# Performance work log

Hardware: AMD Instinct MI355X
Metric: run time of the kernel (lower is better)

Reference implementation:

```python
import jax, jax.numpy as jnp
import numpy as np

N, E, G = 50000, 800000, 64          # nodes, edges, graphs
IN, HID, OUT, H = 256, 64, 64, 4     # input dim, per-head hidden, output dim, heads
NEG_SLOPE = 0.2                      # PyG GATConv leaky_relu slope


def _lin(k, fan_in, fan_out):
    return jax.random.normal(k, (fan_in, fan_out), jnp.float32) * (1.0 / np.sqrt(fan_in))


def setup_inputs() -> dict:
    key = jax.random.key(0)
    ks = jax.random.split(key, 16)
    x = jax.random.normal(ks[0], (N, IN), jnp.float32)
    edge_index = jax.random.randint(ks[1], (2, E), 0, N, dtype=jnp.int32)
    batch = jnp.sort(jax.random.randint(ks[2], (N,), 0, G, dtype=jnp.int32))
    # layer 1: IN -> H x HID (concat)
    W1 = _lin(ks[3], IN, H * HID)
    a_src1 = jax.random.normal(ks[4], (H, HID), jnp.float32) * 0.1
    a_dst1 = jax.random.normal(ks[5], (H, HID), jnp.float32) * 0.1
    b1 = jnp.zeros((H * HID,), jnp.float32)
    # layer 2: H*HID -> H x HID (concat)
    W2 = _lin(ks[6], H * HID, H * HID)
    a_src2 = jax.random.normal(ks[7], (H, HID), jnp.float32) * 0.1
    a_dst2 = jax.random.normal(ks[8], (H, HID), jnp.float32) * 0.1
    b2 = jnp.zeros((H * HID,), jnp.float32)
    W3 = _lin(ks[9], H * HID, OUT)
    a_src3 = jax.random.normal(ks[10], (1, OUT), jnp.float32) * 0.1
    a_dst3 = jax.random.normal(ks[11], (1, OUT), jnp.float32) * 0.1
    b3 = jnp.zeros((OUT,), jnp.float32)
    return {"x": x, "edge_index": edge_index, "batch": batch,
            "W1": W1, "a_src1": a_src1, "a_dst1": a_dst1, "b1": b1,
            "W2": W2, "a_src2": a_src2, "a_dst2": a_dst2, "b2": b2,
            "W3": W3, "a_src3": a_src3, "a_dst3": a_dst3, "b3": b3}


def gat_conv(x, src, dst, W, a_src, a_dst, b, heads, out_ch):
    """PyG-style GATConv (eval mode, concat=True semantics; heads=1 == no concat)."""
    n = x.shape[0]
    h = (x @ W).reshape(n, heads, out_ch)                     # [N,H,C]
    alpha_s = jnp.sum(h * a_src, axis=-1)                     # [N,H]
    alpha_d = jnp.sum(h * a_dst, axis=-1)                     # [N,H]
    e = jax.nn.leaky_relu(alpha_s[src] + alpha_d[dst], NEG_SLOPE)  # [E',H]
    # segment softmax over destination nodes (self-loops guarantee nonempty segments)
    m = jax.ops.segment_max(e, dst, num_segments=n)
    e = jnp.exp(e - m[dst])
    denom = jax.ops.segment_sum(e, dst, num_segments=n)
    alpha = e / (denom[dst] + 1e-16)                          # [E',H]
    msg = h[src] * alpha[:, :, None]                          # [E',H,C]
    out = jax.ops.segment_sum(msg, dst, num_segments=n)       # [N,H,C]
    return out.reshape(n, heads * out_ch) + b


def reference(x, edge_index, batch, W1, a_src1, a_dst1, b1, W2, a_src2, a_dst2, b2,
              W3, a_src3, a_dst3, b3):
    n = x.shape[0]
    # GATConv default add_self_loops=True
    loops = jnp.arange(n, dtype=edge_index.dtype)
    src = jnp.concatenate([edge_index[0], loops])
    dst = jnp.concatenate([edge_index[1], loops])

    h = gat_conv(x, src, dst, W1, a_src1, a_dst1, b1, H, HID)
    h = jax.nn.elu(h)  # dropout disabled in eval
    h = gat_conv(h, src, dst, W2, a_src2, a_dst2, b2, H, HID)
    h = jax.nn.elu(h)
    node_embeddings = gat_conv(h, src, dst, W3, a_src3, a_dst3, b3, 1, OUT)

    # global_mean_pool over batch ids
    sums = jax.ops.segment_sum(node_embeddings, batch, num_segments=G)
    counts = jax.ops.segment_sum(jnp.ones((n,), node_embeddings.dtype), batch, num_segments=G)
    graph_embeddings = sums / jnp.maximum(counts, 1.0)[:, None]
    return node_embeddings, graph_embeddings
```

## Files before the change

### kernel.cpp

```cpp
#include <hip/hip_runtime.h>
#include <hip/hip_bf16.h>
#include <hip/hip_fp16.h>

typedef __attribute__((ext_vector_type(8))) _Float16 f16x8;
typedef __attribute__((ext_vector_type(4))) _Float16 f16x4;
typedef __attribute__((ext_vector_type(4))) float f32x4;

static __device__ __forceinline__ void st(float* p, float v)  { *p = v; }
static __device__ __forceinline__ void st(__half* p, float v) { *p = __float2half(v); }

static __device__ __forceinline__ void splitf16(float v, __half& hi, __half& lo) {
    hi = __float2half(v);
    lo = __float2half(v - __half2float(hi));
}

__global__ void k_hist(const int* __restrict__ ei, int* deg, int E) {
    int e = blockIdx.x * blockDim.x + threadIdx.x;
    if (e < E) atomicAdd(&deg[ei[E + e]], 1);
}

__global__ void k_scan1(const int* __restrict__ deg, int* __restrict__ offs,
                        int* __restrict__ bsum, int N) {
    __shared__ int sh[256];
    int i = blockIdx.x * 256 + threadIdx.x;
    int v = (i < N) ? (deg[i] + 1) : 0;
    sh[threadIdx.x] = v;
    __syncthreads();
#pragma unroll
    for (int off = 1; off < 256; off <<= 1) {
        int t = (threadIdx.x >= off) ? sh[threadIdx.x - off] : 0;
        __syncthreads();
        sh[threadIdx.x] += t;
        __syncthreads();
    }
    if (i < N) offs[i] = sh[threadIdx.x] - v;
    if (threadIdx.x == 255) bsum[blockIdx.x] = sh[255];
}

__global__ void k_scan2(int* __restrict__ bsum, int nb) {
    __shared__ int sh[256];
    int v = (threadIdx.x < nb) ? bsum[threadIdx.x] : 0;
    sh[threadIdx.x] = v;
    __syncthreads();
#pragma unroll
    for (int off = 1; off < 256; off <<= 1) {
        int t = (threadIdx.x >= off) ? sh[threadIdx.x - off] : 0;
        __syncthreads();
        sh[threadIdx.x] += t;
        __syncthreads();
    }
    if (threadIdx.x < nb) bsum[threadIdx.x] = sh[threadIdx.x] - v;
    if (threadIdx.x == 255) bsum[nb] = sh[255];
}

__global__ void k_scan3(int* __restrict__ offs, int* __restrict__ cursor,
                        const int* __restrict__ bsum, int N, int nb) {
    int i = blockIdx.x * 256 + threadIdx.x;
    if (i < N) {
        int v = offs[i] + bsum[blockIdx.x];
        offs[i] = v;
        cursor[i] = v;
    }
    if (i == 0) offs[N] = bsum[nb];
}

__global__ void k_scatter_all(const int* __restrict__ ei, int* cursor, int* csr,
                              int E, int N) {
    int e = blockIdx.x * blockDim.x + threadIdx.x;
    if (e < E) {
        int d = ei[E + e];
        int p = atomicAdd(&cursor[d], 1);
        csr[p] = ei[e];
    } else if (e < E + N) {
        int i = e - E;
        int p = atomicAdd(&cursor[i], 1);
        csr[p] = i;
    }
}

__global__ void k_wsplit_all(const float* __restrict__ W1, const float* __restrict__ W2,
                             const float* __restrict__ W3,
                             __half* __restrict__ w1h, __half* __restrict__ w1l,
                             __half* __restrict__ w2h, __half* __restrict__ w2l,
                             __half* __restrict__ w3h, __half* __restrict__ w3l) {
    int idx = blockIdx.x * 256 + threadIdx.x;
    const float* W; __half *Wh, *Wl; int M, base;
    constexpr int K = 256;
    if (idx < 65536)       { W = W1; Wh = w1h; Wl = w1l; M = 256; base = idx; }
    else if (idx < 131072) { W = W2; Wh = w2h; Wl = w2l; M = 256; base = idx - 65536; }
    else if (idx < 147456) { W = W3; Wh = w3h; Wl = w3l; M = 64;  base = idx - 131072; }
    else return;
    int k = base / M, n = base - k * M;
    __half h, l;
    splitf16(W[base], h, l);
    Wh[(size_t)n * K + k] = h;
    Wl[(size_t)n * K + k] = l;
}

__global__ void k_xsplit(const float* __restrict__ x, __half* __restrict__ xh,
                         __half* __restrict__ xl, long n4) {
    long i = (long)blockIdx.x * 256 + threadIdx.x;
    if (i < n4) {
        float4 v = *reinterpret_cast<const float4*>(x + i * 4);
        __half h0, h1, h2, h3, l0, l1, l2, l3;
        splitf16(v.x, h0, l0);
        splitf16(v.y, h1, l1);
        splitf16(v.z, h2, l2);
        splitf16(v.w, h3, l3);
        ushort4 hv = { __half_as_ushort(h0), __half_as_ushort(h1),
                       __half_as_ushort(h2), __half_as_ushort(h3) };
        ushort4 lv = { __half_as_ushort(l0), __half_as_ushort(l1),
                       __half_as_ushort(l2), __half_as_ushort(l3) };
        *reinterpret_cast<ushort4*>(xh + i * 4) = hv;
        *reinterpret_cast<ushort4*>(xl + i * 4) = lv;
    }
}

template <typename ACC>
static __device__ __forceinline__ void alpha_epilogue(
        const ACC& acc, float* ldsf, const float* __restrict__ a_src,
        const float* __restrict__ a_dst, float* __restrict__ als,
        float* __restrict__ ald, __half* __restrict__ C,
        int nrows, int M, int H, int r0, int c0,
        int wr, int wc, int quad, int r, int tid) {
    float ps[4][4], pd[4][4];
#pragma unroll
    for (int tr = 0; tr < 4; ++tr)
#pragma unroll
        for (int i = 0; i < 4; ++i) { ps[tr][i] = 0.f; pd[tr][i] = 0.f; }

#pragma unroll
    for (int tr = 0; tr < 4; ++tr)
#pragma unroll
        for (int tc = 0; tc < 2; ++tc) {
            int col = c0 + wc * 32 + tc * 16 + r;
            float av_s = a_src[col], av_d = a_dst[col];
#pragma unroll
            for (int i = 0; i < 4; ++i) {
                int row = r0 + wr * 64 + tr * 16 + quad * 4 + i;
                __half hv = __float2half(acc[tr][tc][i]);
                float vr = __half2float(hv);
                if (row < nrows) C[(size_t)row * M + col] = hv;
                ps[tr][i] = fmaf(vr, av_s, ps[tr][i]);
                pd[tr][i] = fmaf(vr, av_d, pd[tr][i]);
            }
        }
#pragma unroll
    for (int tr = 0; tr < 4; ++tr)
#pragma unroll
        for (int i = 0; i < 4; ++i) {
            float s = ps[tr][i], d2 = pd[tr][i];
#pragma unroll
            for (int off = 1; off < 16; off <<= 1) {
                s  += __shfl_xor(s,  off, 64);
                d2 += __shfl_xor(d2, off, 64);
            }
            if (r == 0) {
                int lrow = wr * 64 + tr * 16 + quad * 4 + i;
                ldsf[(0 * 2 + wc) * 128 + lrow] = s;
                ldsf[(2 + wc) * 128 + lrow]     = d2;
            }
        }
    __syncthreads();
    int lrow = tid >> 1, which = tid & 1;
    if (lrow < 128) {
        float v = ldsf[(which * 2 + 0) * 128 + lrow] + ldsf[(which * 2 + 1) * 128 + lrow];
        int grow = r0 + lrow;
        if (grow < nrows) {
            float* dst = which ? ald : als;
            dst[(size_t)grow * H + (c0 >> 6)] = v;
        }
    }
}

__global__ __launch_bounds__(256) void k_gemm3(const __half* __restrict__ Ah, const __half* __restrict__ Al,
                                               const __half* __restrict__ Wth, const __half* __restrict__ Wtl,
                                               __half* __restrict__ C, int nrows, int K, int M,
                                               const float* __restrict__ a_src, const float* __restrict__ a_dst,
                                               float* __restrict__ als, float* __restrict__ ald, int H) {
    constexpr int LDA = 40;
    __shared__ __half AH[128 * LDA];
    __shared__ __half AL[128 * LDA];
    __shared__ __half BH[64 * LDA];
    __shared__ __half BL[64 * LDA];

    int tid  = threadIdx.x;
    int lane = tid & 63;
    int wave = tid >> 6;
    int wr = wave & 1, wc = wave >> 1;
    int quad = lane >> 4, r = lane & 15;
    int r0 = blockIdx.x * 128, c0 = blockIdx.y * 64;

    f32x4 acc[4][2];
#pragma unroll
    for (int i = 0; i < 4; ++i)
#pragma unroll
        for (int j = 0; j < 2; ++j) acc[i][j] = (f32x4){0.f, 0.f, 0.f, 0.f};

    for (int kc = 0; kc < K; kc += 32) {
#pragma unroll
        for (int it = 0; it < 2; ++it) {
            int row  = (tid >> 2) + it * 64;
            int kseg = (tid & 3) * 8;
            int gr = r0 + row;
            f16x8 vh = (f16x8)(_Float16)0, vl = (f16x8)(_Float16)0;
            if (gr < nrows) {
                vh = *reinterpret_cast<const f16x8*>(Ah + (size_t)gr * K + kc + kseg);
                vl = *reinterpret_cast<const f16x8*>(Al + (size_t)gr * K + kc + kseg);
            }
            *reinterpret_cast<f16x8*>(&AH[row * LDA + kseg]) = vh;
            *reinterpret_cast<f16x8*>(&AL[row * LDA + kseg]) = vl;
        }
        {
            int n    = tid >> 2;
            int kseg = (tid & 3) * 8;
            *reinterpret_cast<f16x8*>(&BH[n * LDA + kseg]) =
                *reinterpret_cast<const f16x8*>(Wth + (size_t)(c0 + n) * K + kc + kseg);
            *reinterpret_cast<f16x8*>(&BL[n * LDA + kseg]) =
                *reinterpret_cast<const f16x8*>(Wtl + (size_t)(c0 + n) * K + kc + kseg);
        }
        __syncthreads();
        int k0 = quad * 8;
        f16x8 ah[4], al[4], bh[2], bl[2];
#pragma unroll
        for (int tr = 0; tr < 4; ++tr) {
            int row = wr * 64 + tr * 16 + r;
            ah[tr] = *reinterpret_cast<const f16x8*>(&AH[row * LDA + k0]);
            al[tr] = *reinterpret_cast<const f16x8*>(&AL[row * LDA + k0]);
        }
#pragma unroll
        for (int tc = 0; tc < 2; ++tc) {
            int col = wc * 32 + tc * 16 + r;
            bh[tc] = *reinterpret_cast<const f16x8*>(&BH[col * LDA + k0]);
            bl[tc] = *reinterpret_cast<const f16x8*>(&BL[col * LDA + k0]);
        }
#pragma unroll
        for (int tr = 0; tr < 4; ++tr)
#pragma unroll
            for (int tc = 0; tc < 2; ++tc) {
                acc[tr][tc] = __builtin_amdgcn_mfma_f32_16x16x32_f16(ah[tr], bh[tc], acc[tr][tc], 0, 0, 0);
                acc[tr][tc] = __builtin_amdgcn_mfma_f32_16x16x32_f16(ah[tr], bl[tc], acc[tr][tc], 0, 0, 0);
                acc[tr][tc] = __builtin_amdgcn_mfma_f32_16x16x32_f16(al[tr], bh[tc], acc[tr][tc], 0, 0, 0);
            }
        __syncthreads();
    }
    alpha_epilogue(acc, reinterpret_cast<float*>(AH), a_src, a_dst, als, ald, C,
                   nrows, M, H, r0, c0, wr, wc, quad, r, tid);
}

__global__ __launch_bounds__(256) void k_gemm2(const __half* __restrict__ A,
                                               const __half* __restrict__ Wth, const __half* __restrict__ Wtl,
                                               __half* __restrict__ C, int nrows, int K, int M,
                                               const float* __restrict__ a_src, const float* __restrict__ a_dst,
                                               float* __restrict__ als, float* __restrict__ ald, int H) {
    constexpr int LDA = 40;
    __shared__ __half AS[128 * LDA];
    __shared__ __half BH[64 * LDA];
    __shared__ __half BL[64 * LDA];

    int tid  = threadIdx.x;
    int lane = tid & 63;
    int wave = tid >> 6;
    int wr = wave & 1, wc = wave >> 1;
    int quad = lane >> 4, r = lane & 15;
    int r0 = blockIdx.x * 128, c0 = blockIdx.y * 64;

    f32x4 acc[4][2];
#pragma unroll
    for (int i = 0; i < 4; ++i)
#pragma unroll
        for (int j = 0; j < 2; ++j) acc[i][j] = (f32x4){0.f, 0.f, 0.f, 0.f};

    for (int kc = 0; kc < K; kc += 32) {
#pragma unroll
        for (int it = 0; it < 2; ++it) {
            int row  = (tid >> 2) + it * 64;
            int kseg = (tid & 3) * 8;
            int gr = r0 + row;
            f16x8 v = (f16x8)(_Float16)0;
            if (gr < nrows) v = *reinterpret_cast<const f16x8*>(A + (size_t)gr * K + kc + kseg);
            *reinterpret_cast<f16x8*>(&AS[row * LDA + kseg]) = v;
        }
        {
            int n    = tid >> 2;
            int kseg = (tid & 3) * 8;
            *reinterpret_cast<f16x8*>(&BH[n * LDA + kseg]) =
                *reinterpret_cast<const f16x8*>(Wth + (size_t)(c0 + n) * K + kc + kseg);
            *reinterpret_cast<f16x8*>(&BL[n * LDA + kseg]) =
                *reinterpret_cast<const f16x8*>(Wtl + (size_t)(c0 + n) * K + kc + kseg);
        }
        __syncthreads();
        int k0 = quad * 8;
        f16x8 a[4], bh[2], bl[2];
#pragma unroll
        for (int tr = 0; tr < 4; ++tr) {
            int row = wr * 64 + tr * 16 + r;
            a[tr] = *reinterpret_cast<const f16x8*>(&AS[row * LDA + k0]);
        }
#pragma unroll
        for (int tc = 0; tc < 2; ++tc) {
            int col = wc * 32 + tc * 16 + r;
            bh[tc] = *reinterpret_cast<const f16x8*>(&BH[col * LDA + k0]);
            bl[tc] = *reinterpret_cast<const f16x8*>(&BL[col * LDA + k0]);
        }
#pragma unroll
        for (int tr = 0; tr < 4; ++tr)
#pragma unroll
            for (int tc = 0; tc < 2; ++tc) {
                acc[tr][tc] = __builtin_amdgcn_mfma_f32_16x16x32_f16(a[tr], bh[tc], acc[tr][tc], 0, 0, 0);
                acc[tr][tc] = __builtin_amdgcn_mfma_f32_16x16x32_f16(a[tr], bl[tc], acc[tr][tc], 0, 0, 0);
            }
        __syncthreads();
    }
    alpha_epilogue(acc, reinterpret_cast<float*>(AS), a_src, a_dst, als, ald, C,
                   nrows, M, H, r0, c0, wr, wc, quad, r, tid);
}

template <int CHUNK, bool ELU, typename OT>
__global__ void k_agg(const __half* __restrict__ feat, const int* __restrict__ offs,
                      const int* __restrict__ csr, const float* __restrict__ als,
                      const float* __restrict__ ald, const float* __restrict__ bias,
                      OT* __restrict__ out, int N) {
    constexpr int M  = 64 * CHUNK;
    constexpr int H  = (CHUNK == 4) ? 4 : 1;
    constexpr int EC = 16;
    constexpr int SH = (CHUNK == 4) ? 9 : 7;

    __shared__ float    shw[4][2][64];
    __shared__ unsigned sho[4][2][EC];

    int tid  = threadIdx.x;
    int lane = tid & 63;
    int wid  = tid >> 6;
    int node = blockIdx.x * 4 + wid;
    if (node >= N) return;

    int ia = lane & 15;
    int ha = (H == 4) ? (lane >> 4) : 0;
    int ho = lane >> 4;

    float adv = ald[(size_t)node * H + ha];

    int beg = offs[node], end = offs[node + 1];
    int d   = end - beg;
    int nc  = (d + EC - 1) >> 4;

    const char* fbase = reinterpret_cast<const char*>(feat) + lane * (CHUNK * 2);

    float acc[CHUNK] = {};
    float den = 0.f;

    int sv = csr[beg + min(ia, min(EC, d) - 1)];
    float xv = als[(size_t)sv * H + ha];
    int sv_n = sv;
    if (nc > 1) {
        int cn = min(EC, d - EC);
        sv_n = csr[beg + EC + min(ia, cn - 1)];
    }

    for (int c = 0; c < nc; ++c) {
        int cnt = min(EC, d - c * EC);

        float e = xv + adv;
        e = (e > 0.f) ? e : 0.2f * e;
        float w = (ia < cnt) ? __expf(e) : 0.f;
        den += w;
        int b = c & 1;
        shw[wid][b][lane] = w;
        if (lane < EC) sho[wid][b][lane] = (unsigned)sv << SH;

        xv = als[(size_t)sv_n * H + ha];
        sv = sv_n;
        if (c + 2 < nc) {
            int cn = min(EC, d - (c + 2) * EC);
            sv_n = csr[beg + (c + 2) * EC + min(ia, cn - 1)];
        }

        const float* wp = &shw[wid][b][ho * EC];
        float4 w0 = *reinterpret_cast<const float4*>(wp);
        float4 w1 = *reinterpret_cast<const float4*>(wp + 4);
        float4 w2 = *reinterpret_cast<const float4*>(wp + 8);
        float4 w3 = *reinterpret_cast<const float4*>(wp + 12);
        const unsigned* op = &sho[wid][b][0];
        uint4 o0 = *reinterpret_cast<const uint4*>(op);
        uint4 o1 = *reinterpret_cast<const uint4*>(op + 4);
        uint4 o2 = *reinterpret_cast<const uint4*>(op + 8);
        uint4 o3 = *reinterpret_cast<const uint4*>(op + 12);
        float    ww[EC] = {w0.x, w0.y, w0.z, w0.w, w1.x, w1.y, w1.z, w1.w,
                           w2.x, w2.y, w2.z, w2.w, w3.x, w3.y, w3.z, w3.w};
        unsigned oo[EC] = {o0.x, o0.y, o0.z, o0.w, o1.x, o1.y, o1.z, o1.w,
                           o2.x, o2.y, o2.z, o2.w, o3.x, o3.y, o3.z, o3.w};
        if constexpr (CHUNK == 4) {
            f16x4 v[EC];
#pragma unroll
            for (int t = 0; t < EC; ++t)
                v[t] = *reinterpret_cast<const f16x4*>(fbase + oo[t]);
#pragma unroll
            for (int t = 0; t < EC; ++t)
#pragma unroll
                for (int j = 0; j < 4; ++j)
                    acc[j] = fmaf((float)v[t][j], ww[t], acc[j]);
        } else {
            __half v[EC];
#pragma unroll
            for (int t = 0; t < EC; ++t)
                v[t] = *reinterpret_cast<const __half*>(fbase + oo[t]);
#pragma unroll
            for (int t = 0; t < EC; ++t)
                acc[0] = fmaf(__half2float(v[t]), ww[t], acc[0]);
        }
    }

#pragma unroll
    for (int off = 1; off < EC; off <<= 1) den += __shfl_xor(den, off, 64);
    float inv = 1.f / (den + 1e-16f);

#pragma unroll
    for (int j = 0; j < CHUNK; ++j) {
        int col = lane * CHUNK + j;
        float v = acc[j] * inv + bias[col];
        if (ELU) v = (v > 0.f) ? v : (__expf(v) - 1.f);
        st(&out[(size_t)node * M + col], v);
    }
}

static __device__ __forceinline__ int lowerb(const int* __restrict__ a, int n, int v) {
    int lo = 0, hi = n;
    while (lo < hi) { int mid = (lo + hi) >> 1; if (a[mid] < v) lo = mid + 1; else hi = mid; }
    return lo;
}

__global__ void k_pool2(const float* __restrict__ ne, const int* __restrict__ batch,
                        float* __restrict__ gout, int N) {
    int g = blockIdx.x;
    int lo = lowerb(batch, N, g);
    int hi = lowerb(batch, N, g + 1);
    int lane = threadIdx.x & 63, row = threadIdx.x >> 6;
    float s = 0.f;
    for (int i = lo + row; i < hi; i += 4) s += ne[(size_t)i * 64 + lane];
    __shared__ float red[4][64];
    red[row][lane] = s;
    __syncthreads();
    if (row == 0) {
        float v = red[0][lane] + red[1][lane] + red[2][lane] + red[3][lane];
        gout[(size_t)g * 64 + lane] = v / fmaxf((float)(hi - lo), 1.f);
    }
}

extern "C" void kernel_launch(void* const* d_in, const int* in_sizes, int n_in,
                              void* d_out, int out_size, void* d_ws, size_t ws_size,
                              hipStream_t stream) {
    const float* x   = (const float*)d_in[0];
    const int* ei    = (const int*)d_in[1];
    const int* batch = (const int*)d_in[2];
    const float* W1  = (const float*)d_in[3];
    const float* as1 = (const float*)d_in[4];
    const float* ad1 = (const float*)d_in[5];
    const float* b1  = (const float*)d_in[6];
    const float* W2  = (const float*)d_in[7];
    const float* as2 = (const float*)d_in[8];
    const float* ad2 = (const float*)d_in[9];
    const float* b2  = (const float*)d_in[10];
    const float* W3  = (const float*)d_in[11];
    const float* as3 = (const float*)d_in[12];
    const float* ad3 = (const float*)d_in[13];
    const float* b3  = (const float*)d_in[14];

    const int N = in_sizes[2];
    const int E = in_sizes[1] / 2;
    const int G = 64;
    float* out = (float*)d_out;

    char* w = (char*)d_ws;
    auto carve = [&](size_t bytes) { char* p = w; w += (bytes + 255) & ~(size_t)255; return p; };
    __half* feat = (__half*)carve((size_t)N * 256 * 2);
    __half* xh   = (__half*)carve((size_t)N * 256 * 2);
    __half* xl   = (__half*)carve((size_t)N * 256 * 2);
    __half* act  = xh;
    float* als   = (float*)carve((size_t)N * 4 * 4);
    float* ald   = (float*)carve((size_t)N * 4 * 4);
    int* deg     = (int*)carve((size_t)N * 4);
    int* offs    = (int*)carve((size_t)(N + 1) * 4);
    int* cursor  = (int*)carve((size_t)N * 4);
    int* csr     = (int*)carve((size_t)(E + N) * 4);
    int nb       = (N + 255) / 256;
    int* bsum    = (int*)carve((size_t)(nb + 1) * 4);
    __half* w1h  = (__half*)carve((size_t)256 * 256 * 2);
    __half* w1l  = (__half*)carve((size_t)256 * 256 * 2);
    __half* w2h  = (__half*)carve((size_t)256 * 256 * 2);
    __half* w2l  = (__half*)carve((size_t)256 * 256 * 2);
    __half* w3h  = (__half*)carve((size_t)256 * 64 * 2);
    __half* w3l  = (__half*)carve((size_t)256 * 64 * 2);

    hipMemsetAsync(deg, 0, (size_t)N * 4, stream);
    k_hist<<<(E + 255) / 256, 256, 0, stream>>>(ei, deg, E);
    k_scan1<<<nb, 256, 0, stream>>>(deg, offs, bsum, N);
    k_scan2<<<1, 256, 0, stream>>>(bsum, nb);
    k_scan3<<<nb, 256, 0, stream>>>(offs, cursor, bsum, N, nb);
    k_scatter_all<<<(E + N + 255) / 256, 256, 0, stream>>>(ei, cursor, csr, E, N);

    k_wsplit_all<<<(147456 + 255) / 256, 256, 0, stream>>>(W1, W2, W3, w1h, w1l, w2h, w2l, w3h, w3l);
    long n4 = (long)N * 64;
    k_xsplit<<<(int)((n4 + 255) / 256), 256, 0, stream>>>(x, xh, xl, n4);

    dim3 gemmBig((N + 127) / 128, 4);
    dim3 gemmSmall((N + 127) / 128, 1);
    int nodeBlocks = (N + 3) / 4;

    k_gemm3<<<gemmBig, 256, 0, stream>>>(xh, xl, w1h, w1l, feat, N, 256, 256,
                                         as1, ad1, als, ald, 4);
    k_agg<4, true, __half><<<nodeBlocks, 256, 0, stream>>>(feat, offs, csr, als, ald, b1, act, N);
    k_gemm2<<<gemmBig, 256, 0, stream>>>(act, w2h, w2l, feat, N, 256, 256,
                                         as2, ad2, als, ald, 4);
    k_agg<4, true, __half><<<nodeBlocks, 256, 0, stream>>>(feat, offs, csr, als, ald, b2, act, N);
    k_gemm2<<<gemmSmall, 256, 0, stream>>>(act, w3h, w3l, feat, N, 256, 64,
                                           as3, ad3, als, ald, 1);
    k_agg<1, false, float><<<nodeBlocks, 256, 0, stream>>>(feat, offs, csr, als, ald, b3, out, N);

    k_pool2<<<G, 256, 0, stream>>>(out, batch, out + (size_t)N * 64, N);
}
```

Before: 541.0 us.

## Fuse preprocessing kernels and overlap CSR scatter with first GEMM

Merges the degree histogram, x split and weight split into one launch. The histogram now records each edge's rank within its destination node, so the CSR scatter needs no second atomic pass. The scatter is moved into the first GEMM launch, where blocks are interleaved as one GEMM block to two scatter blocks, and self-loops are written during the scan. This removes several kernel launches and serial stages, at the cost of an extra rank array, and the block interleaving may unbalance the GEMM launch.

New measurement: 497.1 us. -8.1%, faster.

```diff
diff --git a/kernel.cpp b/kernel.cpp
--- a/kernel.cpp
+++ b/kernel.cpp
@@ -14,76 +14,44 @@
     lo = __float2half(v - __half2float(hi));
 }
 
-__global__ void k_hist(const int* __restrict__ ei, int* deg, int E) {
-    int e = blockIdx.x * blockDim.x + threadIdx.x;
-    if (e < E) atomicAdd(&deg[ei[E + e]], 1);
-}
-
-__global__ void k_scan1(const int* __restrict__ deg, int* __restrict__ offs,
-                        int* __restrict__ bsum, int N) {
-    __shared__ int sh[256];
-    int i = blockIdx.x * 256 + threadIdx.x;
-    int v = (i < N) ? (deg[i] + 1) : 0;
-    sh[threadIdx.x] = v;
-    __syncthreads();
-#pragma unroll
-    for (int off = 1; off < 256; off <<= 1) {
-        int t = (threadIdx.x >= off) ? sh[threadIdx.x - off] : 0;
-        __syncthreads();
-        sh[threadIdx.x] += t;
-        __syncthreads();
-    }
-    if (i < N) offs[i] = sh[threadIdx.x] - v;
-    if (threadIdx.x == 255) bsum[blockIdx.x] = sh[255];
-}
-
-__global__ void k_scan2(int* __restrict__ bsum, int nb) {
-    __shared__ int sh[256];
-    int v = (threadIdx.x < nb) ? bsum[threadIdx.x] : 0;
-    sh[threadIdx.x] = v;
-    __syncthreads();
-#pragma unroll
-    for (int off = 1; off < 256; off <<= 1) {
-        int t = (threadIdx.x >= off) ? sh[threadIdx.x - off] : 0;
-        __syncthreads();
-        sh[threadIdx.x] += t;
-        __syncthreads();
-    }
-    if (threadIdx.x < nb) bsum[threadIdx.x] = sh[threadIdx.x] - v;
-    if (threadIdx.x == 255) bsum[nb] = sh[255];
-}
-
-__global__ void k_scan3(int* __restrict__ offs, int* __restrict__ cursor,
-                        const int* __restrict__ bsum, int N, int nb) {
-    int i = blockIdx.x * 256 + threadIdx.x;
-    if (i < N) {
-        int v = offs[i] + bsum[blockIdx.x];
-        offs[i] = v;
-        cursor[i] = v;
-    }
-    if (i == 0) offs[N] = bsum[nb];
-}
-
-__global__ void k_scatter_all(const int* __restrict__ ei, int* cursor, int* csr,
-                              int E, int N) {
-    int e = blockIdx.x * blockDim.x + threadIdx.x;
-    if (e < E) {
-        int d = ei[E + e];
-        int p = atomicAdd(&cursor[d], 1);
-        csr[p] = ei[e];
-    } else if (e < E + N) {
-        int i = e - E;
-        int p = atomicAdd(&cursor[i], 1);
-        csr[p] = i;
-    }
-}
-
-__global__ void k_wsplit_all(const float* __restrict__ W1, const float* __restrict__ W2,
-                             const float* __restrict__ W3,
-                             __half* __restrict__ w1h, __half* __restrict__ w1l,
-                             __half* __restrict__ w2h, __half* __restrict__ w2l,
-                             __half* __restrict__ w3h, __half* __restrict__ w3l) {
-    int idx = blockIdx.x * 256 + threadIdx.x;
+__global__ void k_pre(const int* __restrict__ ei, int* __restrict__ deg, int* __restrict__ rnk,
+                      int E,
+                      const float* __restrict__ x, __half* __restrict__ xh,
+                      __half* __restrict__ xl, long n4,
+                      const float* __restrict__ W1, const float* __restrict__ W2,
+                      const float* __restrict__ W3,
+                      __half* __restrict__ w1h, __half* __restrict__ w1l,
+                      __half* __restrict__ w2h, __half* __restrict__ w2l,
+                      __half* __restrict__ w3h, __half* __restrict__ w3l) {
+    int bx = blockIdx.x;
+    int nhist = (E + 255) >> 8;
+    if (bx < nhist) {
+        int e = bx * 256 + threadIdx.x;
+        if (e < E) rnk[e] = atomicAdd(&deg[ei[E + e]], 1);
+        return;
+    }
+    bx -= nhist;
+    int nx4 = (int)((n4 + 255) >> 8);
+    if (bx < nx4) {
+        long i = (long)bx * 256 + threadIdx.x;
+        if (i < n4) {
+            float4 v = *reinterpret_cast<const float4*>(x + i * 4);
+            __half h0, h1, h2, h3, l0, l1, l2, l3;
+            splitf16(v.x, h0, l0);
+            splitf16(v.y, h1, l1);
+            splitf16(v.z, h2, l2);
+            splitf16(v.w, h3, l3);
+            ushort4 hv = { __half_as_ushort(h0), __half_as_ushort(h1),
+                           __half_as_ushort(h2), __half_as_ushort(h3) };
+            ushort4 lv = { __half_as_ushort(l0), __half_as_ushort(l1),
+                           __half_as_ushort(l2), __half_as_ushort(l3) };
+            *reinterpret_cast<ushort4*>(xh + i * 4) = hv;
+            *reinterpret_cast<ushort4*>(xl + i * 4) = lv;
+        }
+        return;
+    }
+    bx -= nx4;
+    int idx = bx * 256 + threadIdx.x;
     const float* W; __half *Wh, *Wl; int M, base;
     constexpr int K = 256;
     if (idx < 65536)       { W = W1; Wh = w1h; Wl = w1l; M = 256; base = idx; }
@@ -97,23 +65,50 @@
     Wl[(size_t)n * K + k] = l;
 }
 
-__global__ void k_xsplit(const float* __restrict__ x, __half* __restrict__ xh,
-                         __half* __restrict__ xl, long n4) {
-    long i = (long)blockIdx.x * 256 + threadIdx.x;
-    if (i < n4) {
-        float4 v = *reinterpret_cast<const float4*>(x + i * 4);
-        __half h0, h1, h2, h3, l0, l1, l2, l3;
-        splitf16(v.x, h0, l0);
-        splitf16(v.y, h1, l1);
-        splitf16(v.z, h2, l2);
-        splitf16(v.w, h3, l3);
-        ushort4 hv = { __half_as_ushort(h0), __half_as_ushort(h1),
-                       __half_as_ushort(h2), __half_as_ushort(h3) };
-        ushort4 lv = { __half_as_ushort(l0), __half_as_ushort(l1),
-                       __half_as_ushort(l2), __half_as_ushort(l3) };
-        *reinterpret_cast<ushort4*>(xh + i * 4) = hv;
-        *reinterpret_cast<ushort4*>(xl + i * 4) = lv;
-    }
+__global__ void k_scan1(const int* __restrict__ deg, int* __restrict__ offs,
+                        int* __restrict__ bsum, int N) {
+    __shared__ int sh[256];
+    int i = blockIdx.x * 256 + threadIdx.x;
+    int v = (i < N) ? (deg[i] + 1) : 0;
+    sh[threadIdx.x] = v;
+    __syncthreads();
+#pragma unroll
+    for (int off = 1; off < 256; off <<= 1) {
+        int t = (threadIdx.x >= off) ? sh[threadIdx.x - off] : 0;
+        __syncthreads();
+        sh[threadIdx.x] += t;
+        __syncthreads();
+    }
+    if (i < N) offs[i] = sh[threadIdx.x] - v;
+    if (threadIdx.x == 255) bsum[blockIdx.x] = sh[255];
+}
+
+__global__ void k_scan2(int* __restrict__ bsum, int nb) {
+    __shared__ int sh[256];
+    int v = (threadIdx.x < nb) ? bsum[threadIdx.x] : 0;
+    sh[threadIdx.x] = v;
+    __syncthreads();
+#pragma unroll
+    for (int off = 1; off < 256; off <<= 1) {
+        int t = (threadIdx.x >= off) ? sh[threadIdx.x - off] : 0;
+        __syncthreads();
+        sh[threadIdx.x] += t;
+        __syncthreads();
+    }
+    if (threadIdx.x < nb) bsum[threadIdx.x] = sh[threadIdx.x] - v;
+    if (threadIdx.x == 255) bsum[nb] = sh[255];
+}
+
+__global__ void k_scan3(int* __restrict__ offs, const int* __restrict__ deg,
+                        int* __restrict__ csr, const int* __restrict__ bsum,
+                        int N, int nb) {
+    int i = blockIdx.x * 256 + threadIdx.x;
+    if (i < N) {
+        int v = offs[i] + bsum[blockIdx.x];
+        offs[i] = v;
+        csr[v + deg[i]] = i;
+    }
+    if (i == 0) offs[N] = bsum[nb];
 }
 
 template <typename ACC>
@@ -173,23 +168,39 @@
     }
 }
 
-__global__ __launch_bounds__(256) void k_gemm3(const __half* __restrict__ Ah, const __half* __restrict__ Al,
-                                               const __half* __restrict__ Wth, const __half* __restrict__ Wtl,
-                                               __half* __restrict__ C, int nrows, int K, int M,
-                                               const float* __restrict__ a_src, const float* __restrict__ a_dst,
-                                               float* __restrict__ als, float* __restrict__ ald, int H) {
+__global__ __launch_bounds__(256) void k_g3s(const __half* __restrict__ Ah, const __half* __restrict__ Al,
+                                             const __half* __restrict__ Wth, const __half* __restrict__ Wtl,
+                                             __half* __restrict__ C, int nrows, int K, int M,
+                                             const float* __restrict__ a_src, const float* __restrict__ a_dst,
+                                             float* __restrict__ als, float* __restrict__ ald, int H,
+                                             int gridRows, int gemmBlocks,
+                                             const int* __restrict__ ei, const int* __restrict__ rnk,
+                                             const int* __restrict__ offs, int* __restrict__ csr, int E) {
     constexpr int LDA = 40;
     __shared__ __half AH[128 * LDA];
     __shared__ __half AL[128 * LDA];
     __shared__ __half BH[64 * LDA];
     __shared__ __half BL[64 * LDA];
 
+    int gx = blockIdx.x;
+    int g = gx / 3, rsel = gx - g * 3;
+    if (rsel != 0) {
+        int e = (g * 2 + (rsel - 1)) * 256 + threadIdx.x;
+        if (e < E) {
+            int dn = ei[E + e];
+            csr[offs[dn] + rnk[e]] = ei[e];
+        }
+        return;
+    }
+    if (g >= gemmBlocks) return;
+    int bxg = g % gridRows, byg = g / gridRows;
+
     int tid  = threadIdx.x;
     int lane = tid & 63;
     int wave = tid >> 6;
     int wr = wave & 1, wc = wave >> 1;
     int quad = lane >> 4, r = lane & 15;
-    int r0 = blockIdx.x * 128, c0 = blockIdx.y * 64;
+    int r0 = bxg * 128, c0 = byg * 64;
 
     f32x4 acc[4][2];
 #pragma unroll
@@ -481,7 +492,7 @@
     float* ald   = (float*)carve((size_t)N * 4 * 4);
     int* deg     = (int*)carve((size_t)N * 4);
     int* offs    = (int*)carve((size_t)(N + 1) * 4);
-    int* cursor  = (int*)carve((size_t)N * 4);
+    int* rnk     = (int*)carve((size_t)E * 4);
     int* csr     = (int*)carve((size_t)(E + N) * 4);
     int nb       = (N + 255) / 256;
     int* bsum    = (int*)carve((size_t)(nb + 1) * 4);
@@ -492,29 +503,32 @@
     __half* w3h  = (__half*)carve((size_t)256 * 64 * 2);
     __half* w3l  = (__half*)carve((size_t)256 * 64 * 2);
 
+    long n4 = (long)N * 64;
+    int nhist = (E + 255) / 256;
+    int nx4   = (int)((n4 + 255) / 256);
+    int nwspl = (147456 + 255) / 256;
+
     hipMemsetAsync(deg, 0, (size_t)N * 4, stream);
-    k_hist<<<(E + 255) / 256, 256, 0, stream>>>(ei, deg, E);
+    k_pre<<<nhist + nx4 + nwspl, 256, 0, stream>>>(ei, deg, rnk, E, x, xh, xl, n4,
+                                                   W1, W2, W3, w1h, w1l, w2h, w2l, w3h, w3l);
+
     k_scan1<<<nb, 256, 0, stream>>>(deg, offs, bsum, N);
     k_scan2<<<1, 256, 0, stream>>>(bsum, nb);
-    k_scan3<<<nb, 256, 0, stream>>>(offs, cursor, bsum, N, nb);
-    k_scatter_all<<<(E + N + 255) / 256, 256, 0, stream>>>(ei, cursor, csr, E, N);
-
-    k_wsplit_all<<<(147456 + 255) / 256, 256, 0, stream>>>(W1, W2, W3, w1h, w1l, w2h, w2l, w3h, w3l);
-    long n4 = (long)N * 64;
-    k_xsplit<<<(int)((n4 + 255) / 256), 256, 0, stream>>>(x, xh, xl, n4);
-
-    dim3 gemmBig((N + 127) / 128, 4);
-    dim3 gemmSmall((N + 127) / 128, 1);
+    k_scan3<<<nb, 256, 0, stream>>>(offs, deg, csr, bsum, N, nb);
+
+    int gridRows = (N + 127) / 128;
+    int gemmBlocks = gridRows * 4;
     int nodeBlocks = (N + 3) / 4;
 
-    k_gemm3<<<gemmBig, 256, 0, stream>>>(xh, xl, w1h, w1l, feat, N, 256, 256,
-                                         as1, ad1, als, ald, 4);
+    k_g3s<<<3 * gemmBlocks, 256, 0, stream>>>(xh, xl, w1h, w1l, feat, N, 256, 256,
+                                              as1, ad1, als, ald, 4,
+                                              gridRows, gemmBlocks, ei, rnk, offs, csr, E);
     k_agg<4, true, __half><<<nodeBlocks, 256, 0, stream>>>(feat, offs, csr, als, ald, b1, act, N);
-    k_gemm2<<<gemmBig, 256, 0, stream>>>(act, w2h, w2l, feat, N, 256, 256,
-                                         as2, ad2, als, ald, 4);
+    k_gemm2<<<dim3(gridRows, 4), 256, 0, stream>>>(act, w2h, w2l, feat, N, 256, 256,
+                                                   as2, ad2, als, ald, 4);
     k_agg<4, true, __half><<<nodeBlocks, 256, 0, stream>>>(feat, offs, csr, als, ald, b2, act, N);
-    k_gemm2<<<gemmSmall, 256, 0, stream>>>(act, w3h, w3l, feat, N, 256, 64,
-                                           as3, ad3, als, ald, 1);
+    k_gemm2<<<dim3(gridRows, 1), 256, 0, stream>>>(act, w3h, w3l, feat, N, 256, 64,
+                                                   as3, ad3, als, ald, 1);
     k_agg<1, false, float><<<nodeBlocks, 256, 0, stream>>>(feat, offs, csr, als, ald, b3, out, N);
 
     k_pool2<<<G, 256, 0, stream>>>(out, batch, out + (size_t)N * 64, N);
```
